# Optimization experiments

Measured on AMD Instinct MI355X. Metric: run time of the kernel, lower is better.

## Reference

```python
import jax, jax.numpy as jnp
import numpy as np

B = 8192      # n_trials
N = 4096      # network size
N_IN = 3      # input channels (1 osc + 2 stim)
TAU = 0.1
DT = 0.0005


def setup_inputs() -> dict:
    key = jax.random.key(0)
    ks = jax.random.split(key, 8)
    k_t = jax.random.normal(ks[0], (B, 2), dtype=jnp.float32)
    phase = jax.random.uniform(ks[1], (B,), dtype=jnp.float32) * 2.0 * np.pi
    monodromy = jnp.tile(jnp.eye(2, dtype=jnp.float32)[None], (B, 1, 1))
    dK_norms = jnp.zeros((B,), dtype=jnp.float32)
    amp = jnp.float32(1.5)
    w = jnp.float32(2.0 * np.pi * 4.0)  # reference oscillation frequency
    stim = jax.random.normal(ks[2], (N_IN - 1,), dtype=jnp.float32)
    alpha = jax.random.normal(ks[3], (2, N_IN), dtype=jnp.float32)
    I = jax.random.normal(ks[4], (N_IN, N), dtype=jnp.float32)
    m = jax.random.normal(ks[5], (2, N), dtype=jnp.float32)
    n = jax.random.normal(ks[6], (2, N), dtype=jnp.float32)
    return {"k_t": k_t, "phase": phase, "monodromy": monodromy,
            "dK_norms": dK_norms, "amp": amp, "w": w, "stim": stim,
            "alpha": alpha, "I": I, "m": m, "n": n}


def reference(k_t, phase, monodromy, dK_norms, amp, w, stim, alpha, I, m, n):
    # calc_x_u
    tau_sw = w * TAU
    v_osc = amp / jnp.sqrt(1.0 + tau_sw ** 2) * jnp.sin(phase - jnp.arctan2(tau_sw, 1.0))  # [B]
    u_osc = amp * jnp.sin(phase)                                                           # [B]
    u_stim = jnp.broadcast_to(stim[None, :], (phase.shape[0], stim.shape[0]))              # [B, n_in-1]
    u = jnp.concatenate([u_osc[:, None], u_stim], axis=-1)                                  # [B, n_in]
    v = jnp.concatenate([v_osc[:, None], u_stim], axis=-1)                                  # [B, n_in]
    x = k_t @ m + v @ I                                                                     # [B, N]
    tx = jnp.tanh(x)
    # dKdt
    dK = (1.0 / TAU) * (-k_t + tx @ n.T / N + u @ alpha.T)                                  # [B, 2]
    # Jacobian: (1/tau) * (-I2 + (1/N) * einsum over neurons)
    dphi = 1.0 - tx ** 2                                                                    # [B, N]
    Jac = (1.0 / TAU) * (-jnp.eye(2, dtype=x.dtype)[None]
                         + jnp.einsum('bn,kn,dn->bkd', dphi, m, n) / N)                     # [B, 2, 2]
    # Euler update
    k_out = k_t + DT * dK
    phase_out = phase + DT * w
    mono_out = monodromy + DT * jnp.einsum('bkd,bde->bke', Jac, monodromy)
    dK_norms_out = dK_norms + jnp.linalg.norm(dK, axis=-1)
    return (k_out, phase_out, mono_out, dK_norms_out)
```

## Files before the change

kernel.cpp:

```cpp
#include <hip/hip_runtime.h>
#include <math.h>

#define N_SIZE 4096
#define B_SIZE 8192
#define T_PER_WAVE 4

__device__ __forceinline__ float fast_tanh(float x) {
    float xe = fminf(x * 2.885390081777927f, 80.0f);
    float e  = __builtin_amdgcn_exp2f(xe);
    return 1.0f - 2.0f * __builtin_amdgcn_rcpf(e + 1.0f);
}

__device__ __forceinline__ float wave_sum(float v) {
#pragma unroll
    for (int off = 32; off >= 1; off >>= 1)
        v += __shfl_xor(v, off, 64);
    return v;
}

__global__ __launch_bounds__(256)
void bif_kernel(const float* __restrict__ k_t,
                const float* __restrict__ phase,
                const float* __restrict__ mono,
                const float* __restrict__ dKn,
                const float* __restrict__ amp_p,
                const float* __restrict__ w_p,
                const float* __restrict__ stim,
                const float* __restrict__ alpha,
                const float* __restrict__ Im,
                const float* __restrict__ mm,
                const float* __restrict__ nm,
                float* __restrict__ out) {
    const int lane = threadIdx.x & 63;
    const int wave = (blockIdx.x * 256 + threadIdx.x) >> 6;
    const int b0   = wave * T_PER_WAVE;

    const float amp = amp_p[0];
    const float w   = w_p[0];
    const float st0 = stim[0];
    const float st1 = stim[1];
    const float tau_sw = w * 0.1f;
    const float phi0 = atanf(tau_sw);
    const float vamp = amp / sqrtf(1.0f + tau_sw * tau_sw);

    float k0[T_PER_WAVE], k1[T_PER_WAVE], vo[T_PER_WAVE], uo[T_PER_WAVE], ph[T_PER_WAVE];
#pragma unroll
    for (int t = 0; t < T_PER_WAVE; ++t) {
        int b = b0 + t;
        k0[t] = k_t[2 * b];
        k1[t] = k_t[2 * b + 1];
        float p = phase[b];
        ph[t] = p;
        vo[t] = vamp * sinf(p - phi0);
        uo[t] = amp * sinf(p);
    }

    float acc_s0[T_PER_WAVE] = {}, acc_s1[T_PER_WAVE] = {};
    float acc00[T_PER_WAVE] = {}, acc01[T_PER_WAVE] = {};
    float acc10[T_PER_WAVE] = {}, acc11[T_PER_WAVE] = {};

    for (int it = 0; it < N_SIZE / 256; ++it) {
        const int j = it * 1024 + lane * 4;
        float4 vm0 = *(const float4*)(mm + j);
        float4 vm1 = *(const float4*)(mm + N_SIZE + j);
        float4 vn0 = *(const float4*)(nm + j);
        float4 vn1 = *(const float4*)(nm + N_SIZE + j);
        float4 vi0 = *(const float4*)(Im + j);
        float4 vi1 = *(const float4*)(Im + N_SIZE + j);
        float4 vi2 = *(const float4*)(Im + 2 * N_SIZE + j);
        const float* pm0 = (const float*)&vm0;
        const float* pm1 = (const float*)&vm1;
        const float* pn0 = (const float*)&vn0;
        const float* pn1 = (const float*)&vn1;
        const float* pi0 = (const float*)&vi0;
        const float* pi1 = (const float*)&vi1;
        const float* pi2 = (const float*)&vi2;
#pragma unroll
        for (int e = 0; e < 4; ++e) {
            const float M0 = pm0[e], M1 = pm1[e];
            const float Nv0 = pn0[e], Nv1 = pn1[e];
            const float I0 = pi0[e];
            const float cv = fmaf(st0, pi1[e], st1 * pi2[e]);
#pragma unroll
            for (int t = 0; t < T_PER_WAVE; ++t) {
                float x  = fmaf(k0[t], M0, fmaf(k1[t], M1, fmaf(vo[t], I0, cv)));
                float tx = fast_tanh(x);
                acc_s0[t] = fmaf(tx, Nv0, acc_s0[t]);
                acc_s1[t] = fmaf(tx, Nv1, acc_s1[t]);
                float dphi = fmaf(-tx, tx, 1.0f);
                float a0 = dphi * M0;
                float a1 = dphi * M1;
                acc00[t] = fmaf(a0, Nv0, acc00[t]);
                acc01[t] = fmaf(a0, Nv1, acc01[t]);
                acc10[t] = fmaf(a1, Nv0, acc10[t]);
                acc11[t] = fmaf(a1, Nv1, acc11[t]);
            }
        }
    }

#pragma unroll
    for (int t = 0; t < T_PER_WAVE; ++t) {
        acc_s0[t] = wave_sum(acc_s0[t]);
        acc_s1[t] = wave_sum(acc_s1[t]);
        acc00[t]  = wave_sum(acc00[t]);
        acc01[t]  = wave_sum(acc01[t]);
        acc10[t]  = wave_sum(acc10[t]);
        acc11[t]  = wave_sum(acc11[t]);
    }

    if (lane == 0) {
        const float a00 = alpha[0], a01 = alpha[1], a02 = alpha[2];
        const float a10 = alpha[3], a11 = alpha[4], a12 = alpha[5];
        const float invN = 1.0f / 4096.0f;
        const float DT = 0.0005f;
#pragma unroll
        for (int t = 0; t < T_PER_WAVE; ++t) {
            const int b = b0 + t;
            float ua0 = uo[t] * a00 + st0 * a01 + st1 * a02;
            float ua1 = uo[t] * a10 + st0 * a11 + st1 * a12;
            float dK0 = 10.0f * (-k0[t] + acc_s0[t] * invN + ua0);
            float dK1 = 10.0f * (-k1[t] + acc_s1[t] * invN + ua1);
            out[2 * b]     = fmaf(DT, dK0, k0[t]);
            out[2 * b + 1] = fmaf(DT, dK1, k1[t]);
            out[B_SIZE * 2 + b] = ph[t] + DT * w;
            float J00 = 10.0f * (acc00[t] * invN - 1.0f);
            float J01 = 10.0f * (acc01[t] * invN);
            float J10 = 10.0f * (acc10[t] * invN);
            float J11 = 10.0f * (acc11[t] * invN - 1.0f);
            float M00 = mono[4 * b], M01 = mono[4 * b + 1];
            float M10 = mono[4 * b + 2], M11 = mono[4 * b + 3];
            float* om = out + B_SIZE * 3 + 4 * b;
            om[0] = M00 + DT * (J00 * M00 + J01 * M10);
            om[1] = M01 + DT * (J00 * M01 + J01 * M11);
            om[2] = M10 + DT * (J10 * M00 + J11 * M10);
            om[3] = M11 + DT * (J10 * M01 + J11 * M11);
            out[B_SIZE * 7 + b] = dKn[b] + sqrtf(dK0 * dK0 + dK1 * dK1);
        }
    }
}

extern "C" void kernel_launch(void* const* d_in, const int* in_sizes, int n_in,
                              void* d_out, int out_size, void* d_ws, size_t ws_size,
                              hipStream_t stream) {
    const float* k_t   = (const float*)d_in[0];
    const float* phase = (const float*)d_in[1];
    const float* mono  = (const float*)d_in[2];
    const float* dKn   = (const float*)d_in[3];
    const float* amp   = (const float*)d_in[4];
    const float* w     = (const float*)d_in[5];
    const float* stim  = (const float*)d_in[6];
    const float* alpha = (const float*)d_in[7];
    const float* Im    = (const float*)d_in[8];
    const float* mm    = (const float*)d_in[9];
    const float* nm    = (const float*)d_in[10];
    float* out = (float*)d_out;

    const int blocks = B_SIZE / (T_PER_WAVE * 4);
    bif_kernel<<<blocks, 256, 0, stream>>>(k_t, phase, mono, dKn, amp, w,
                                           stim, alpha, Im, mm, nm, out);
}
```

Before: 27.75 us.

## Stage weight vectors in LDS per half and use packed float2 math

The per-neuron weight rows (m, n, I and a precomputed stim contribution) are now staged into shared memory in two halves by 512-thread blocks, and the waves read them from LDS instead of global/L2. The stim term is precomputed once per element rather than per wave. The inner loop uses 2-wide vector types to encourage packed FP32 instructions, and the batch items per wave drop from 4 to 2, with launch bounds raised for occupancy. The costs are added barriers and less reuse of each loaded weight across batch items. The tanh input clamp is also removed, so very large inputs could overflow exp2.

```diff
diff --git a/kernel.cpp b/kernel.cpp
--- a/kernel.cpp
+++ b/kernel.cpp
@@ -3,13 +3,10 @@
 
 #define N_SIZE 4096
 #define B_SIZE 8192
-#define T_PER_WAVE 4
+#define NH 2048
+#define T_PER_WAVE 2
 
-__device__ __forceinline__ float fast_tanh(float x) {
-    float xe = fminf(x * 2.885390081777927f, 80.0f);
-    float e  = __builtin_amdgcn_exp2f(xe);
-    return 1.0f - 2.0f * __builtin_amdgcn_rcpf(e + 1.0f);
-}
+typedef float v2f __attribute__((ext_vector_type(2)));
 
 __device__ __forceinline__ float wave_sum(float v) {
 #pragma unroll
@@ -18,7 +15,19 @@
     return v;
 }
 
-__global__ __launch_bounds__(256)
+__device__ __forceinline__ v2f tanh2(v2f x) {
+    v2f xe = x * 2.885390081777927f;
+    v2f ex;
+    ex.x = __builtin_amdgcn_exp2f(xe.x);
+    ex.y = __builtin_amdgcn_exp2f(xe.y);
+    v2f d = ex + 1.0f;
+    v2f r;
+    r.x = __builtin_amdgcn_rcpf(d.x);
+    r.y = __builtin_amdgcn_rcpf(d.y);
+    return 1.0f - 2.0f * r;
+}
+
+__global__ __launch_bounds__(512, 4)
 void bif_kernel(const float* __restrict__ k_t,
                 const float* __restrict__ phase,
                 const float* __restrict__ mono,
@@ -31,9 +40,11 @@
                 const float* __restrict__ mm,
                 const float* __restrict__ nm,
                 float* __restrict__ out) {
+    __shared__ float s_m0[NH], s_m1[NH], s_n0[NH], s_n1[NH], s_I0[NH], s_cv[NH];
+
     const int lane = threadIdx.x & 63;
-    const int wave = (blockIdx.x * 256 + threadIdx.x) >> 6;
-    const int b0   = wave * T_PER_WAVE;
+    const int wid  = threadIdx.x >> 6;
+    const int b0   = (blockIdx.x * 8 + wid) * T_PER_WAVE;
 
     const float amp = amp_p[0];
     const float w   = w_p[0];
@@ -55,78 +66,91 @@
         uo[t] = amp * sinf(p);
     }
 
-    float acc_s0[T_PER_WAVE] = {}, acc_s1[T_PER_WAVE] = {};
-    float acc00[T_PER_WAVE] = {}, acc01[T_PER_WAVE] = {};
-    float acc10[T_PER_WAVE] = {}, acc11[T_PER_WAVE] = {};
+    v2f As0[T_PER_WAVE] = {}, As1[T_PER_WAVE] = {};
+    v2f A00[T_PER_WAVE] = {}, A01[T_PER_WAVE] = {};
+    v2f A10[T_PER_WAVE] = {}, A11[T_PER_WAVE] = {};
 
-    for (int it = 0; it < N_SIZE / 256; ++it) {
-        const int j = it * 1024 + lane * 4;
-        float4 vm0 = *(const float4*)(mm + j);
-        float4 vm1 = *(const float4*)(mm + N_SIZE + j);
-        float4 vn0 = *(const float4*)(nm + j);
-        float4 vn1 = *(const float4*)(nm + N_SIZE + j);
-        float4 vi0 = *(const float4*)(Im + j);
-        float4 vi1 = *(const float4*)(Im + N_SIZE + j);
-        float4 vi2 = *(const float4*)(Im + 2 * N_SIZE + j);
-        const float* pm0 = (const float*)&vm0;
-        const float* pm1 = (const float*)&vm1;
-        const float* pn0 = (const float*)&vn0;
-        const float* pn1 = (const float*)&vn1;
-        const float* pi0 = (const float*)&vi0;
-        const float* pi1 = (const float*)&vi1;
-        const float* pi2 = (const float*)&vi2;
+    for (int half = 0; half < 2; ++half) {
+        {
+            const int t4 = threadIdx.x * 4;
+            const int g  = half * NH + t4;
+            *(float4*)&s_m0[t4] = *(const float4*)&mm[g];
+            *(float4*)&s_m1[t4] = *(const float4*)&mm[N_SIZE + g];
+            *(float4*)&s_n0[t4] = *(const float4*)&nm[g];
+            *(float4*)&s_n1[t4] = *(const float4*)&nm[N_SIZE + g];
+            *(float4*)&s_I0[t4] = *(const float4*)&Im[g];
+            float4 i1 = *(const float4*)&Im[N_SIZE + g];
+            float4 i2 = *(const float4*)&Im[2 * N_SIZE + g];
+            float4 cv;
+            cv.x = st0 * i1.x + st1 * i2.x;
+            cv.y = st0 * i1.y + st1 * i2.y;
+            cv.z = st0 * i1.z + st1 * i2.z;
+            cv.w = st0 * i1.w + st1 * i2.w;
+            *(float4*)&s_cv[t4] = cv;
+        }
+        __syncthreads();
+
+#pragma unroll 2
+        for (int it = 0; it < NH / 256; ++it) {
+            const int j = it * 256 + lane * 4;
+            float4 fm0 = *(const float4*)&s_m0[j];
+            float4 fm1 = *(const float4*)&s_m1[j];
+            float4 fn0 = *(const float4*)&s_n0[j];
+            float4 fn1 = *(const float4*)&s_n1[j];
+            float4 fi0 = *(const float4*)&s_I0[j];
+            float4 fcv = *(const float4*)&s_cv[j];
+            v2f Ms0[2] = {{fm0.x, fm0.y}, {fm0.z, fm0.w}};
+            v2f Ms1[2] = {{fm1.x, fm1.y}, {fm1.z, fm1.w}};
+            v2f Nn0[2] = {{fn0.x, fn0.y}, {fn0.z, fn0.w}};
+            v2f Nn1[2] = {{fn1.x, fn1.y}, {fn1.z, fn1.w}};
+            v2f Iv[2]  = {{fi0.x, fi0.y}, {fi0.z, fi0.w}};
+            v2f Cv[2]  = {{fcv.x, fcv.y}, {fcv.z, fcv.w}};
 #pragma unroll
-        for (int e = 0; e < 4; ++e) {
-            const float M0 = pm0[e], M1 = pm1[e];
-            const float Nv0 = pn0[e], Nv1 = pn1[e];
-            const float I0 = pi0[e];
-            const float cv = fmaf(st0, pi1[e], st1 * pi2[e]);
+            for (int p = 0; p < 2; ++p) {
 #pragma unroll
-            for (int t = 0; t < T_PER_WAVE; ++t) {
-                float x  = fmaf(k0[t], M0, fmaf(k1[t], M1, fmaf(vo[t], I0, cv)));
-                float tx = fast_tanh(x);
-                acc_s0[t] = fmaf(tx, Nv0, acc_s0[t]);
-                acc_s1[t] = fmaf(tx, Nv1, acc_s1[t]);
-                float dphi = fmaf(-tx, tx, 1.0f);
-                float a0 = dphi * M0;
-                float a1 = dphi * M1;
-                acc00[t] = fmaf(a0, Nv0, acc00[t]);
-                acc01[t] = fmaf(a0, Nv1, acc01[t]);
-                acc10[t] = fmaf(a1, Nv0, acc10[t]);
-                acc11[t] = fmaf(a1, Nv1, acc11[t]);
+                for (int t = 0; t < T_PER_WAVE; ++t) {
+                    v2f x  = Cv[p] + k0[t] * Ms0[p] + k1[t] * Ms1[p] + vo[t] * Iv[p];
+                    v2f tx = tanh2(x);
+                    v2f dphi = 1.0f - tx * tx;
+                    v2f a0 = dphi * Ms0[p];
+                    v2f a1 = dphi * Ms1[p];
+                    As0[t] += tx * Nn0[p];
+                    As1[t] += tx * Nn1[p];
+                    A00[t] += a0 * Nn0[p];
+                    A01[t] += a0 * Nn1[p];
+                    A10[t] += a1 * Nn0[p];
+                    A11[t] += a1 * Nn1[p];
+                }
             }
         }
+        __syncthreads();
     }
 
+    const float a00 = alpha[0], a01 = alpha[1], a02 = alpha[2];
+    const float a10 = alpha[3], a11 = alpha[4], a12 = alpha[5];
+    const float invN = 1.0f / 4096.0f;
+    const float DT = 0.0005f;
 #pragma unroll
     for (int t = 0; t < T_PER_WAVE; ++t) {
-        acc_s0[t] = wave_sum(acc_s0[t]);
-        acc_s1[t] = wave_sum(acc_s1[t]);
-        acc00[t]  = wave_sum(acc00[t]);
-        acc01[t]  = wave_sum(acc01[t]);
-        acc10[t]  = wave_sum(acc10[t]);
-        acc11[t]  = wave_sum(acc11[t]);
-    }
-
-    if (lane == 0) {
-        const float a00 = alpha[0], a01 = alpha[1], a02 = alpha[2];
-        const float a10 = alpha[3], a11 = alpha[4], a12 = alpha[5];
-        const float invN = 1.0f / 4096.0f;
-        const float DT = 0.0005f;
-#pragma unroll
-        for (int t = 0; t < T_PER_WAVE; ++t) {
+        float s0  = wave_sum(As0[t].x + As0[t].y);
+        float s1  = wave_sum(As1[t].x + As1[t].y);
+        float j00 = wave_sum(A00[t].x + A00[t].y);
+        float j01 = wave_sum(A01[t].x + A01[t].y);
+        float j10 = wave_sum(A10[t].x + A10[t].y);
+        float j11 = wave_sum(A11[t].x + A11[t].y);
+        if (lane == 0) {
             const int b = b0 + t;
             float ua0 = uo[t] * a00 + st0 * a01 + st1 * a02;
             float ua1 = uo[t] * a10 + st0 * a11 + st1 * a12;
-            float dK0 = 10.0f * (-k0[t] + acc_s0[t] * invN + ua0);
-            float dK1 = 10.0f * (-k1[t] + acc_s1[t] * invN + ua1);
+            float dK0 = 10.0f * (-k0[t] + s0 * invN + ua0);
+            float dK1 = 10.0f * (-k1[t] + s1 * invN + ua1);
             out[2 * b]     = fmaf(DT, dK0, k0[t]);
             out[2 * b + 1] = fmaf(DT, dK1, k1[t]);
             out[B_SIZE * 2 + b] = ph[t] + DT * w;
-            float J00 = 10.0f * (acc00[t] * invN - 1.0f);
-            float J01 = 10.0f * (acc01[t] * invN);
-            float J10 = 10.0f * (acc10[t] * invN);
-            float J11 = 10.0f * (acc11[t] * invN - 1.0f);
+            float J00 = 10.0f * (j00 * invN - 1.0f);
+            float J01 = 10.0f * (j01 * invN);
+            float J10 = 10.0f * (j10 * invN);
+            float J11 = 10.0f * (j11 * invN - 1.0f);
             float M00 = mono[4 * b], M01 = mono[4 * b + 1];
             float M10 = mono[4 * b + 2], M11 = mono[4 * b + 3];
             float* om = out + B_SIZE * 3 + 4 * b;
@@ -155,7 +179,6 @@
     const float* nm    = (const float*)d_in[10];
     float* out = (float*)d_out;
 
-    const int blocks = B_SIZE / (T_PER_WAVE * 4);
-    bif_kernel<<<blocks, 256, 0, stream>>>(k_t, phase, mono, dKn, amp, w,
-                                           stim, alpha, Im, mm, nm, out);
+    bif_kernel<<<B_SIZE / (8 * T_PER_WAVE), 512, 0, stream>>>(
+        k_t, phase, mono, dKn, amp, w, stim, alpha, Im, mm, nm, out);
 }
```

Measured after the change: 25.15 us. -9.4%, faster.
